# Performance work log

Measured on AMD Instinct MI355X. Metric: run time of the kernel, lower is better.

## Reference

```python
import jax, jax.numpy as jnp
import numpy as np

N, D, E, K = 16384, 512, 8, 2  # tokens, model dim, experts, top_k


def setup_inputs() -> dict:
    key = jax.random.key(0)
    k_x, k_l, k_w = jax.random.split(key, 3)
    input_batch = jax.random.normal(k_x, (N, D), dtype=jnp.float32)
    # Router-like top-k gates: distinct expert ids per token (matches the
    # module's assumption that each (token, slot) maps to a unique expert row).
    logits = jax.random.normal(k_l, (N, E), dtype=jnp.float32)
    top_vals, top_idx = jax.lax.top_k(logits, K)
    probabilities = jax.nn.softmax(top_vals, axis=-1)          # [N, K]
    indices = top_idx.astype(jnp.int32)                        # [N, K]
    W = jax.random.normal(k_w, (E, D, D), dtype=jnp.float32) * (1.0 / np.sqrt(D))
    b = jnp.zeros((E, D), dtype=jnp.float32)
    return {"input_batch": input_batch, "probabilities": probabilities,
            "indices": indices, "W": W, "b": b}


def reference(input_batch, probabilities, indices, W, b):
    # Original loops over experts, gathers tokens routed to each expert,
    # runs the expert, concatenates, restores original (token, slot) order,
    # applies AFTER_EXPERTS gate weighting, and sums over the top_k slots.
    # Equivalent vectorized math: out[n] = sum_k p[n,k] * expert_{idx[n,k]}(x[n]).
    y = jnp.einsum('nd,edo->eno', input_batch, W) + b[:, None, :]   # [E, N, D]
    n_ar = jnp.arange(input_batch.shape[0])[:, None]                # [N, 1]
    gathered = y[indices, n_ar]                                     # [N, K, D]
    output = jnp.sum(probabilities[..., None] * gathered, axis=1)   # [N, D]
    total_loss = jnp.float32(0.0)  # sampler_loss=0 (external indices), expert losses=0
    return output, total_loss
```

## Files before the change

### kernel.cpp

```cpp
#include <hip/hip_runtime.h>

#define NTOK 16384
#define DIM  512
#define NEXP 8
#define NPAIR 64
#define PCAP 8192

#define BM 128
#define BN 64
#define BK 32

typedef __bf16 bf16x8 __attribute__((ext_vector_type(8)));
typedef __bf16 bf16x4 __attribute__((ext_vector_type(4)));
typedef float  f32x4  __attribute__((ext_vector_type(4)));

__device__ __forceinline__ void async_cp16(const void* g, void* l) {
    __builtin_amdgcn_global_load_lds((const __attribute__((address_space(1))) void*)g,
                                     (__attribute__((address_space(3))) void*)l, 16, 0, 0);
}

__global__ __launch_bounds__(256) void k_prep(const float* __restrict__ W,
                                              __bf16* __restrict__ Wt,
                                              const float* __restrict__ x,
                                              __bf16* __restrict__ xb,
                                              const int* __restrict__ indices,
                                              const float* __restrict__ probs,
                                              int* __restrict__ cnt,
                                              int* __restrict__ tok_arr,
                                              float* __restrict__ plo_arr,
                                              float* __restrict__ phi_arr,
                                              float* __restrict__ out) {
    int b = blockIdx.x, tid = threadIdx.x;
    if (b < 2048) {
        __shared__ __bf16 tile[32][34];
        int e = b >> 8, rem = b & 255;
        int o0 = (rem >> 4) * 32, k0 = (rem & 15) * 32;
        const float* Wsrc = W + ((size_t)e * DIM + k0) * DIM + o0;
        for (int i = tid; i < 1024; i += 256) {
            int kk = i >> 5, oo = i & 31;
            tile[oo][kk] = (__bf16)Wsrc[(size_t)kk * DIM + oo];
        }
        __syncthreads();
        __bf16* dst = Wt + ((size_t)(e * 16 + (k0 >> 5)) * DIM + o0) * 32;
        for (int i = tid; i < 1024; i += 256) {
            int oo = i >> 5, kk = i & 31;
            dst[oo * 32 + kk] = tile[oo][kk];
        }
    } else if (b < 2304) {
        int base = (b - 2048) * 256 + tid;
        const float4* src = (const float4*)x;
        #pragma unroll
        for (int it = 0; it < 32; ++it) {
            int i = base + it * 65536;
            float4 v = src[i];
            bf16x4 h; h[0] = (__bf16)v.x; h[1] = (__bf16)v.y; h[2] = (__bf16)v.z; h[3] = (__bf16)v.w;
            *(bf16x4*)&xb[(size_t)i * 4] = h;
        }
    } else {
        __shared__ int lcnt[NPAIR], lbase[NPAIR];
        int t = (b - 2304) * 256 + tid;
        if (tid < NPAIR) lcnt[tid] = 0;
        __syncthreads();
        int   e0 = indices[2 * t], e1 = indices[2 * t + 1];
        float p0 = probs[2 * t],   p1 = probs[2 * t + 1];
        int lo = min(e0, e1), hi = max(e0, e1);
        float plo = (e0 < e1) ? p0 : p1;
        float phi = (e0 < e1) ? p1 : p0;
        int key = lo * 8 + hi;
        int lr = atomicAdd(&lcnt[key], 1);
        __syncthreads();
        if (tid < NPAIR) lbase[tid] = atomicAdd(&cnt[tid], lcnt[tid]);
        __syncthreads();
        int pos = lbase[key] + lr;
        if (pos < PCAP) {
            int q = key * PCAP + pos;
            tok_arr[q] = t; plo_arr[q] = plo; phi_arr[q] = phi;
        }
        if (b == 2304 && tid == 0) out[NTOK * DIM] = 0.0f;
    }
}

__global__ __launch_bounds__(256) void k_gemm(const __bf16* __restrict__ xb,
                                              const __bf16* __restrict__ Wt,
                                              const float* __restrict__ bias,
                                              const int* __restrict__ tok_arr,
                                              const float* __restrict__ plo_arr,
                                              const float* __restrict__ phi_arr,
                                              const int* __restrict__ cnt,
                                              float* __restrict__ out) {
    int p = blockIdx.x;
    int r = p & 7;
    int nt = (p >> 3) & 7;
    int m_slot = (p >> 6) * 8 + r;
    int key = -1, m_t = 0, count = 0, total = 0;
    for (int i = 0; i < NPAIR; ++i) {
        int c = cnt[i];
        int tl = (c + BM - 1) >> 7;
        if (key < 0 && m_slot < total + tl) { key = i; m_t = m_slot - total; count = c; }
        total += tl;
    }
    if (key < 0) return;
    if (count > PCAP) count = PCAP;
    int lo = key >> 3, hi = key & 7;
    int m0 = m_t * BM, n0 = nt * BN, tid = threadIdx.x;

    __shared__ __attribute__((aligned(16))) char smem[32768];
    __shared__ int   sTok[BM];
    __shared__ float sPlo[BM], sPhi[BM];

    if (tid < BM) {
        int g = m0 + tid;
        int tk = 0; float a = 0.f, h = 0.f;
        if (g < count) {
            int q = key * PCAP + g;
            tk = tok_arr[q]; a = plo_arr[q]; h = phi_arr[q];
        }
        sTok[tid] = tk;
        sPlo[tid] = a; sPhi[tid] = h;
    }
    __syncthreads();

    int wid  = tid >> 6, lane = tid & 63;
    int quad = lane >> 4, rr  = lane & 15;
    int wm = (wid >> 1) * 64, wn = (wid & 1) * 32;

    int rA0 = tid >> 2;
    int swz = ((tid & 3) ^ (rA0 & 3)) << 3;
    const __bf16* gA0 = xb + (size_t)sTok[rA0]      * DIM + swz;
    const __bf16* gA1 = xb + (size_t)sTok[rA0 + 64] * DIM + swz;
    size_t bOff = (size_t)((rA0 * 4 + ((tid & 3) ^ (rA0 & 3))) * 8);
    const __bf16* gBlo = Wt + ((size_t)(lo * 16) * DIM + n0) * 32 + bOff;
    const __bf16* gBhi = Wt + ((size_t)(hi * 16) * DIM + n0) * 32 + bOff;

    f32x4 accL[4][2] = {};
    f32x4 accH[4][2] = {};

    async_cp16(gA0,  smem + tid * 16);
    async_cp16(gA1,  smem + tid * 16 + 4096);
    async_cp16(gBlo, smem + 16384 + tid * 16);
    async_cp16(gBhi, smem + 24576 + tid * 16);

    #pragma unroll 2
    for (int kt = 0; kt < 16; ++kt) {
        int cur = kt & 1;
        __syncthreads();
        if (kt < 15) {
            int ka = (kt + 1) * BK;
            size_t wOff = (size_t)(kt + 1) * DIM * 32;
            int nx = (kt + 1) & 1;
            async_cp16(gA0 + ka,    smem + nx * 8192 + tid * 16);
            async_cp16(gA1 + ka,    smem + nx * 8192 + tid * 16 + 4096);
            async_cp16(gBlo + wOff, smem + 16384 + nx * 4096 + tid * 16);
            async_cp16(gBhi + wOff, smem + 24576 + nx * 4096 + tid * 16);
        }
        const __bf16* sA  = (const __bf16*)(smem +         cur * 8192);
        const __bf16* sBl = (const __bf16*)(smem + 16384 + cur * 4096);
        const __bf16* sBh = (const __bf16*)(smem + 24576 + cur * 4096);
        int csw = (quad ^ (rr & 3)) * 8;
        bf16x8 af[4], bl[2], bh[2];
        #pragma unroll
        for (int i = 0; i < 4; ++i)
            af[i] = *(bf16x8*)&sA[(wm + i * 16 + rr) * BK + csw];
        #pragma unroll
        for (int j = 0; j < 2; ++j) {
            bl[j] = *(bf16x8*)&sBl[(wn + j * 16 + rr) * BK + csw];
            bh[j] = *(bf16x8*)&sBh[(wn + j * 16 + rr) * BK + csw];
        }
        #pragma unroll
        for (int i = 0; i < 4; ++i)
            #pragma unroll
            for (int j = 0; j < 2; ++j) {
                accL[i][j] = __builtin_amdgcn_mfma_f32_16x16x32_bf16(af[i], bl[j], accL[i][j], 0, 0, 0);
                accH[i][j] = __builtin_amdgcn_mfma_f32_16x16x32_bf16(af[i], bh[j], accH[i][j], 0, 0, 0);
            }
    }

    float blo[2], bhi[2];
    #pragma unroll
    for (int j = 0; j < 2; ++j) {
        blo[j] = bias[lo * DIM + n0 + wn + j * 16 + rr];
        bhi[j] = bias[hi * DIM + n0 + wn + j * 16 + rr];
    }
    #pragma unroll
    for (int i = 0; i < 4; ++i) {
        #pragma unroll
        for (int reg = 0; reg < 4; ++reg) {
            int row = wm + i * 16 + quad * 4 + reg;
            int g = m0 + row;
            if (g >= count) continue;
            int   tk = sTok[row];
            float pl = sPlo[row], ph = sPhi[row];
            float* dst = out + (size_t)tk * DIM + n0 + wn + rr;
            #pragma unroll
            for (int j = 0; j < 2; ++j)
                dst[j * 16] = accL[i][j][reg] * pl + accH[i][j][reg] * ph + pl * blo[j] + ph * bhi[j];
        }
    }
}

extern "C" void kernel_launch(void* const* d_in, const int* in_sizes, int n_in,
                              void* d_out, int out_size, void* d_ws, size_t ws_size,
                              hipStream_t stream) {
    const float* x    = (const float*)d_in[0];
    const float* prob = (const float*)d_in[1];
    const int*   idx  = (const int*)d_in[2];
    const float* W    = (const float*)d_in[3];
    const float* b    = (const float*)d_in[4];
    float* out = (float*)d_out;

    char* ws = (char*)d_ws;
    __bf16* Wt      = (__bf16*)ws;
    __bf16* xb      = (__bf16*)(ws + 4194304);
    int*    cnt     = (int*)   (ws + 4194304 + 16777216);
    int*    tok_arr = (int*)   (ws + 4194304 + 16777216 + 256);
    float*  plo_arr = (float*) (ws + 4194304 + 16777216 + 256 + 2097152);
    float*  phi_arr = (float*) (ws + 4194304 + 16777216 + 256 + 2 * 2097152);

    (void)hipMemsetAsync(cnt, 0, NPAIR * sizeof(int), stream);
    hipLaunchKernelGGL(k_prep, dim3(2368), dim3(256), 0, stream,
                       W, Wt, x, xb, idx, prob, cnt, tok_arr, plo_arr, phi_arr, out);
    hipLaunchKernelGGL(k_gemm, dim3(1280), dim3(256), 0, stream,
                       xb, Wt, b, tok_arr, plo_arr, phi_arr, cnt, out);
}
```

Baseline: 139.0 us.

## Fuse fp32-to-bf16 activation conversion into GEMM A-tile load path

Removes the separate pass in the prep kernel that converted the whole input to bf16 in workspace. The GEMM now async-copies fp32 activation rows straight into shared memory with a new swizzle and converts them to bf16 when building MFMA fragments. This drops a 32MB read plus 16MB write pass. In exchange the A tile traffic per GEMM doubles (fp32 gathers, repeated across the 8 N-tiles), shared memory grows to 48KB which may cut occupancy, and conversion work is added inside the inner loop.

```diff
diff --git a/kernel.cpp b/kernel.cpp
--- a/kernel.cpp
+++ b/kernel.cpp
@@ -21,8 +21,6 @@
 
 __global__ __launch_bounds__(256) void k_prep(const float* __restrict__ W,
                                               __bf16* __restrict__ Wt,
-                                              const float* __restrict__ x,
-                                              __bf16* __restrict__ xb,
                                               const int* __restrict__ indices,
                                               const float* __restrict__ probs,
                                               int* __restrict__ cnt,
@@ -46,19 +44,9 @@
             int oo = i >> 5, kk = i & 31;
             dst[oo * 32 + kk] = tile[oo][kk];
         }
-    } else if (b < 2304) {
-        int base = (b - 2048) * 256 + tid;
-        const float4* src = (const float4*)x;
-        #pragma unroll
-        for (int it = 0; it < 32; ++it) {
-            int i = base + it * 65536;
-            float4 v = src[i];
-            bf16x4 h; h[0] = (__bf16)v.x; h[1] = (__bf16)v.y; h[2] = (__bf16)v.z; h[3] = (__bf16)v.w;
-            *(bf16x4*)&xb[(size_t)i * 4] = h;
-        }
     } else {
         __shared__ int lcnt[NPAIR], lbase[NPAIR];
-        int t = (b - 2304) * 256 + tid;
+        int t = (b - 2048) * 256 + tid;
         if (tid < NPAIR) lcnt[tid] = 0;
         __syncthreads();
         int   e0 = indices[2 * t], e1 = indices[2 * t + 1];
@@ -76,11 +64,11 @@
             int q = key * PCAP + pos;
             tok_arr[q] = t; plo_arr[q] = plo; phi_arr[q] = phi;
         }
-        if (b == 2304 && tid == 0) out[NTOK * DIM] = 0.0f;
-    }
-}
-
-__global__ __launch_bounds__(256) void k_gemm(const __bf16* __restrict__ xb,
+        if (b == 2048 && tid == 0) out[NTOK * DIM] = 0.0f;
+    }
+}
+
+__global__ __launch_bounds__(256) void k_gemm(const float* __restrict__ x,
                                               const __bf16* __restrict__ Wt,
                                               const float* __restrict__ bias,
                                               const int* __restrict__ tok_arr,
@@ -104,7 +92,7 @@
     int lo = key >> 3, hi = key & 7;
     int m0 = m_t * BM, n0 = nt * BN, tid = threadIdx.x;
 
-    __shared__ __attribute__((aligned(16))) char smem[32768];
+    __shared__ __attribute__((aligned(16))) char smem[49152];
     __shared__ int   sTok[BM];
     __shared__ float sPlo[BM], sPhi[BM];
 
@@ -124,11 +112,14 @@
     int quad = lane >> 4, rr  = lane & 15;
     int wm = (wid >> 1) * 64, wn = (wid & 1) * 32;
 
-    int rA0 = tid >> 2;
-    int swz = ((tid & 3) ^ (rA0 & 3)) << 3;
-    const __bf16* gA0 = xb + (size_t)sTok[rA0]      * DIM + swz;
-    const __bf16* gA1 = xb + (size_t)sTok[rA0 + 64] * DIM + swz;
-    size_t bOff = (size_t)((rA0 * 4 + ((tid & 3) ^ (rA0 & 3))) * 8);
+    int rA   = tid >> 3;
+    int qc   = ((((tid >> 1) & 3) ^ (rA & 3)) << 1) | (tid & 1);
+    const float* gA0 = x + (size_t)sTok[rA]      * DIM + qc * 4;
+    const float* gA1 = x + (size_t)sTok[rA + 32] * DIM + qc * 4;
+    const float* gA2 = x + (size_t)sTok[rA + 64] * DIM + qc * 4;
+    const float* gA3 = x + (size_t)sTok[rA + 96] * DIM + qc * 4;
+    int rB = tid >> 2;
+    size_t bOff = (size_t)((rB * 4 + ((tid & 3) ^ (rB & 3))) * 8);
     const __bf16* gBlo = Wt + ((size_t)(lo * 16) * DIM + n0) * 32 + bOff;
     const __bf16* gBhi = Wt + ((size_t)(hi * 16) * DIM + n0) * 32 + bOff;
 
@@ -137,8 +128,10 @@
 
     async_cp16(gA0,  smem + tid * 16);
     async_cp16(gA1,  smem + tid * 16 + 4096);
-    async_cp16(gBlo, smem + 16384 + tid * 16);
-    async_cp16(gBhi, smem + 24576 + tid * 16);
+    async_cp16(gA2,  smem + tid * 16 + 8192);
+    async_cp16(gA3,  smem + tid * 16 + 12288);
+    async_cp16(gBlo, smem + 32768 + tid * 16);
+    async_cp16(gBhi, smem + 40960 + tid * 16);
 
     #pragma unroll 2
     for (int kt = 0; kt < 16; ++kt) {
@@ -148,19 +141,28 @@
             int ka = (kt + 1) * BK;
             size_t wOff = (size_t)(kt + 1) * DIM * 32;
             int nx = (kt + 1) & 1;
-            async_cp16(gA0 + ka,    smem + nx * 8192 + tid * 16);
-            async_cp16(gA1 + ka,    smem + nx * 8192 + tid * 16 + 4096);
-            async_cp16(gBlo + wOff, smem + 16384 + nx * 4096 + tid * 16);
-            async_cp16(gBhi + wOff, smem + 24576 + nx * 4096 + tid * 16);
-        }
-        const __bf16* sA  = (const __bf16*)(smem +         cur * 8192);
-        const __bf16* sBl = (const __bf16*)(smem + 16384 + cur * 4096);
-        const __bf16* sBh = (const __bf16*)(smem + 24576 + cur * 4096);
+            char* dA = smem + nx * 16384;
+            async_cp16(gA0 + ka,    dA + tid * 16);
+            async_cp16(gA1 + ka,    dA + tid * 16 + 4096);
+            async_cp16(gA2 + ka,    dA + tid * 16 + 8192);
+            async_cp16(gA3 + ka,    dA + tid * 16 + 12288);
+            async_cp16(gBlo + wOff, smem + 32768 + nx * 4096 + tid * 16);
+            async_cp16(gBhi + wOff, smem + 40960 + nx * 4096 + tid * 16);
+        }
+        const char*   sA  = smem + cur * 16384;
+        const __bf16* sBl = (const __bf16*)(smem + 32768 + cur * 4096);
+        const __bf16* sBh = (const __bf16*)(smem + 40960 + cur * 4096);
+        bf16x8 af[4], bl[2], bh[2];
+        #pragma unroll
+        for (int i = 0; i < 4; ++i) {
+            int row = wm + i * 16 + rr;
+            int off = row * 128 + ((quad ^ (row & 3)) * 32);
+            f32x4 a0 = *(const f32x4*)(sA + off);
+            f32x4 a1 = *(const f32x4*)(sA + off + 16);
+            #pragma unroll
+            for (int k = 0; k < 4; ++k) { af[i][k] = (__bf16)a0[k]; af[i][4 + k] = (__bf16)a1[k]; }
+        }
         int csw = (quad ^ (rr & 3)) * 8;
-        bf16x8 af[4], bl[2], bh[2];
-        #pragma unroll
-        for (int i = 0; i < 4; ++i)
-            af[i] = *(bf16x8*)&sA[(wm + i * 16 + rr) * BK + csw];
         #pragma unroll
         for (int j = 0; j < 2; ++j) {
             bl[j] = *(bf16x8*)&sBl[(wn + j * 16 + rr) * BK + csw];
@@ -210,15 +212,14 @@
 
     char* ws = (char*)d_ws;
     __bf16* Wt      = (__bf16*)ws;
-    __bf16* xb      = (__bf16*)(ws + 4194304);
-    int*    cnt     = (int*)   (ws + 4194304 + 16777216);
-    int*    tok_arr = (int*)   (ws + 4194304 + 16777216 + 256);
-    float*  plo_arr = (float*) (ws + 4194304 + 16777216 + 256 + 2097152);
-    float*  phi_arr = (float*) (ws + 4194304 + 16777216 + 256 + 2 * 2097152);
+    int*    cnt     = (int*)   (ws + 4194304);
+    int*    tok_arr = (int*)   (ws + 4194304 + 256);
+    float*  plo_arr = (float*) (ws + 4194304 + 256 + 2097152);
+    float*  phi_arr = (float*) (ws + 4194304 + 256 + 2 * 2097152);
 
     (void)hipMemsetAsync(cnt, 0, NPAIR * sizeof(int), stream);
-    hipLaunchKernelGGL(k_prep, dim3(2368), dim3(256), 0, stream,
-                       W, Wt, x, xb, idx, prob, cnt, tok_arr, plo_arr, phi_arr, out);
+    hipLaunchKernelGGL(k_prep, dim3(2112), dim3(256), 0, stream,
+                       W, Wt, idx, prob, cnt, tok_arr, plo_arr, phi_arr, out);
     hipLaunchKernelGGL(k_gemm, dim3(1280), dim3(256), 0, stream,
-                       xb, Wt, b, tok_arr, plo_arr, phi_arr, cnt, out);
-}
+                       x, Wt, b, tok_arr, plo_arr, phi_arr, cnt, out);
+}
```

Result: slower. 144.8 us (+4.2%).
